# Performance work log

Measured on AMD Instinct MI355X. Metric: run time of the kernel, lower is better.

Reference implementation:

```python
import jax, jax.numpy as jnp
import numpy as np

EMB = 1024
HEADS = 16

def setup_inputs() -> dict:
    key = jax.random.key(0)
    ks = jax.random.split(key, 5)
    s = 1.0 / np.sqrt(EMB)
    x = jax.random.normal(ks[0], (2, 2048, EMB), dtype=jnp.float32)
    W_qkv = jax.random.normal(ks[1], (EMB, 3 * EMB), dtype=jnp.float32) * s
    b_qkv = jnp.zeros((3 * EMB,), dtype=jnp.float32)
    W_out = jax.random.normal(ks[2], (EMB, EMB), dtype=jnp.float32) * s
    b_out = jnp.zeros((EMB,), dtype=jnp.float32)
    return {"x": x, "W_qkv": W_qkv, "b_qkv": b_qkv, "W_out": W_out, "b_out": b_out}

def reference(x, W_qkv, b_qkv, W_out, b_out):
    B, N, C = x.shape
    H = HEADS
    D = C // H
    qkv = x @ W_qkv + b_qkv                      # [B,N,3C]
    qkv = qkv.reshape(B, N, 3, H, D)
    q, k, v = (qkv[:, :, i].transpose(0, 2, 1, 3) for i in range(3))  # [B,H,N,D]
    # NOTE: original scales by C**-0.5 (full embed dim), not head dim
    scale = C ** (-0.5)
    attn = jnp.einsum('bhnd,bhmd->bhnm', q, k) * scale
    attn = jax.nn.softmax(attn, axis=-1)
    out = jnp.einsum('bhnm,bhmd->bhnd', attn, v)  # [B,H,N,D]
    out = out.transpose(0, 2, 1, 3).reshape(B, N, C)
    return out @ W_out + b_out
```

## Files before the change

kernel.cpp:

```cpp
#include <hip/hip_runtime.h>
#include <hip/hip_bf16.h>
#include <cstdint>
#include <cstddef>

typedef __bf16 bf16;
typedef __bf16 bf16x4 __attribute__((ext_vector_type(4)));
typedef __bf16 bf16x8 __attribute__((ext_vector_type(8)));
typedef float f32x4 __attribute__((ext_vector_type(4)));
typedef float f32x16 __attribute__((ext_vector_type(16)));

#define LOG2E 1.4426950408889634f
#define QSCALE (0.03125f * LOG2E)

#define GLD16(gp, lp)                                                              \
  __builtin_amdgcn_global_load_lds((__attribute__((address_space(1))) void*)(gp),  \
                                   (__attribute__((address_space(3))) void*)(lp),  \
                                   16, 0, 0)

__global__ void k_prep(const float* __restrict__ x, const float* __restrict__ Wqkv,
                       const float* __restrict__ Wout, bf16* __restrict__ xb,
                       bf16* __restrict__ wqT, bf16* __restrict__ woT) {
  const int blk = blockIdx.x, tid = threadIdx.x;
  if (blk < 2048) {
    int i = (blk * 256 + tid) * 8;
    const float4* p = (const float4*)(x + i);
    float4 a = p[0], b = p[1];
    bf16x8 o;
    o[0] = (bf16)a.x; o[1] = (bf16)a.y; o[2] = (bf16)a.z; o[3] = (bf16)a.w;
    o[4] = (bf16)b.x; o[5] = (bf16)b.y; o[6] = (bf16)b.z; o[7] = (bf16)b.w;
    *(bf16x8*)(xb + i) = o;
    return;
  }
  const float* in;
  bf16* out;
  int R = 1024, C, bx, by;
  if (blk < 2048 + 3072) {
    in = Wqkv; out = wqT; C = 3072;
    bx = (blk - 2048) % 96; by = (blk - 2048) / 96;
  } else {
    in = Wout; out = woT; C = 1024;
    bx = (blk - 5120) % 32; by = (blk - 5120) / 32;
  }
  __shared__ float t[32][33];
  const int tx = tid & 31, ty = tid >> 5;
  int c0 = bx * 32, r0 = by * 32;
#pragma unroll
  for (int i = 0; i < 4; i++)
    t[ty + i * 8][tx] = in[(size_t)(r0 + ty + i * 8) * C + c0 + tx];
  __syncthreads();
#pragma unroll
  for (int i = 0; i < 4; i++)
    out[(size_t)(c0 + ty + i * 8) * R + r0 + tx] = (bf16)t[tx][ty + i * 8];
}

__global__ __launch_bounds__(256, 3) void k_gemm_qkv(
    const bf16* __restrict__ A, const bf16* __restrict__ Bt,
    const float* __restrict__ bias,
    bf16* __restrict__ qb, bf16* __restrict__ kb, bf16* __restrict__ vb) {
  __shared__ __align__(16) bf16 As[128 * 32];
  __shared__ __align__(16) bf16 Bs[128 * 32];
  const int tid = threadIdx.x;
  const int lane = tid & 63, w = tid >> 6;
  const int quad = lane >> 4, l16 = lane & 15;
  const int wm = (w >> 1) * 64, wn = (w & 1) * 64;
  const int bm = blockIdx.y * 128, bn = blockIdx.x * 128;
  f32x4 acc[4][4] = {};

  for (int kt = 0; kt < 1024; kt += 32) {
    __syncthreads();
#pragma unroll
    for (int p = 0; p < 2; p++) {
      int idx = p * 256 + tid;
      int row = idx >> 2, bq = idx & 3;
      int gb = (bq - ((row >> 1) & 3)) & 3;
      GLD16(A + (size_t)(bm + row) * 1024 + kt + gb * 8, As + idx * 8);
      GLD16(Bt + (size_t)(bn + row) * 1024 + kt + gb * 8, Bs + idx * 8);
    }
    __syncthreads();

    bf16x8 af[4], bfr[4];
#pragma unroll
    for (int mi = 0; mi < 4; mi++) {
      int row = wm + mi * 16 + l16;
      int bq = (quad + ((row >> 1) & 3)) & 3;
      af[mi] = *(const bf16x8*)(As + row * 32 + bq * 8);
    }
#pragma unroll
    for (int ni = 0; ni < 4; ni++) {
      int row = wn + ni * 16 + l16;
      int bq = (quad + ((row >> 1) & 3)) & 3;
      bfr[ni] = *(const bf16x8*)(Bs + row * 32 + bq * 8);
    }
#pragma unroll
    for (int mi = 0; mi < 4; mi++)
#pragma unroll
      for (int ni = 0; ni < 4; ni++)
        acc[mi][ni] =
            __builtin_amdgcn_mfma_f32_16x16x32_bf16(af[mi], bfr[ni], acc[mi][ni], 0, 0, 0);
  }

#pragma unroll
  for (int ni = 0; ni < 4; ni++) {
    int col = bn + wn + ni * 16 + l16;
    float bv = bias[col];
    int which = col >> 10, cc = col & 1023;
    int h = cc >> 6, d = cc & 63;
    if (which == 2) {
#pragma unroll
      for (int mi = 0; mi < 4; mi++) {
        int rowb = bm + wm + mi * 16 + quad * 4;
        int b = rowb >> 11, n0 = rowb & 2047;
        int n0p = (n0 & ~12) | ((n0 & 4) << 1) | ((n0 & 8) >> 1);
        bf16x4 vv;
#pragma unroll
        for (int r = 0; r < 4; r++) vv[r] = (bf16)(acc[mi][ni][r] + bv);
        *(bf16x4*)(vb + ((size_t)(b * 16 + h) * 64 + d) * 2048 + n0p) = vv;
      }
    } else {
#pragma unroll
      for (int mi = 0; mi < 4; mi++)
#pragma unroll
        for (int r = 0; r < 4; r++) {
          int row = bm + wm + mi * 16 + quad * 4 + r;
          int b = row >> 11, n = row & 2047;
          float v = acc[mi][ni][r] + bv;
          if (which == 0)
            qb[((size_t)(b * 16 + h) * 2048 + n) * 64 + d] = (bf16)(v * QSCALE);
          else
            kb[((size_t)(b * 16 + h) * 2048 + n) * 64 + d] = (bf16)v;
        }
    }
  }
}

__global__ __launch_bounds__(256, 2) void k_gemm_out(
    const bf16* __restrict__ A, const bf16* __restrict__ Bt,
    const float* __restrict__ bias, float* __restrict__ outF) {
  __shared__ __align__(16) bf16 As[64 * 32];
  __shared__ __align__(16) bf16 Bs[128 * 32];
  const int tid = threadIdx.x;
  const int lane = tid & 63, w = tid >> 6;
  const int quad = lane >> 4, l16 = lane & 15;
  const int wm = (w >> 1) * 32, wn = (w & 1) * 64;
  const int cid = (blockIdx.x & 7) * 64 + (blockIdx.x >> 3);
  const int bn = (cid & 7) * 128, bm = (cid >> 3) * 64;
  f32x4 acc[2][4] = {};

  for (int kt = 0; kt < 1024; kt += 32) {
    __syncthreads();
    {
      int idx = tid;
      int row = idx >> 2, bq = idx & 3;
      int gb = (bq - ((row >> 1) & 3)) & 3;
      GLD16(A + (size_t)(bm + row) * 1024 + kt + gb * 8, As + idx * 8);
    }
#pragma unroll
    for (int p = 0; p < 2; p++) {
      int idx = p * 256 + tid;
      int row = idx >> 2, bq = idx & 3;
      int gb = (bq - ((row >> 1) & 3)) & 3;
      GLD16(Bt + (size_t)(bn + row) * 1024 + kt + gb * 8, Bs + idx * 8);
    }
    __syncthreads();

    bf16x8 af[2], bfr[4];
#pragma unroll
    for (int mi = 0; mi < 2; mi++) {
      int row = wm + mi * 16 + l16;
      int bq = (quad + ((row >> 1) & 3)) & 3;
      af[mi] = *(const bf16x8*)(As + row * 32 + bq * 8);
    }
#pragma unroll
    for (int ni = 0; ni < 4; ni++) {
      int row = wn + ni * 16 + l16;
      int bq = (quad + ((row >> 1) & 3)) & 3;
      bfr[ni] = *(const bf16x8*)(Bs + row * 32 + bq * 8);
    }
#pragma unroll
    for (int mi = 0; mi < 2; mi++)
#pragma unroll
      for (int ni = 0; ni < 4; ni++)
        acc[mi][ni] =
            __builtin_amdgcn_mfma_f32_16x16x32_bf16(af[mi], bfr[ni], acc[mi][ni], 0, 0, 0);
  }

#pragma unroll
  for (int ni = 0; ni < 4; ni++) {
    int col = bn + wn + ni * 16 + l16;
    float bv = bias[col];
#pragma unroll
    for (int mi = 0; mi < 2; mi++)
#pragma unroll
      for (int r = 0; r < 4; r++) {
        int row = bm + wm + mi * 16 + quad * 4 + r;
        outF[(size_t)row * 1024 + col] = acc[mi][ni][r] + bv;
      }
  }
}

__global__ __launch_bounds__(256, 4) void k_flash(
    const bf16* __restrict__ Q, const bf16* __restrict__ K,
    const bf16* __restrict__ V, bf16* __restrict__ O) {
  __shared__ __align__(16) bf16 Kt[2][64 * 64];
  __shared__ __align__(16) bf16 Vt[2][64 * 64];
  const int tid = threadIdx.x;
  const int lane = tid & 63, w = tid >> 6;
  const int wq = w >> 1, wk = w & 1;
  const int l31 = lane & 31, h = lane >> 5;
  const int x7 = l31 & 7;
  const int cid = ((blockIdx.x & 7) << 7) | (blockIdx.x >> 3);
  const int qt = cid & 31, bh = cid >> 5;
  const bf16* qh = Q + (size_t)bh * 2048 * 64;
  const bf16* kh = K + (size_t)bh * 2048 * 64;
  const bf16* vh = V + (size_t)bh * 64 * 2048;
  const int qrow = qt * 64 + wq * 32 + l31;

  bf16x8 qf[4];
#pragma unroll
  for (int c4 = 0; c4 < 4; c4++)
    qf[c4] = *(const bf16x8*)(qh + (size_t)qrow * 64 + c4 * 16 + h * 8);

  bf16x8 ones;
#pragma unroll
  for (int j = 0; j < 8; j++) ones[j] = (bf16)1.0f;
  f32x16 z16 = {};

  f32x16 o0 = {}, o1 = {};
  f32x16 lacc = {};

  auto stage = [&](int kt2, int buf) {
#pragma unroll
    for (int pp = 0; pp < 2; pp++) {
      int idx = pp * 256 + tid;
      int row = idx >> 3, bq = idx & 7, gb = bq ^ (row & 7);
      GLD16(kh + (size_t)(kt2 * 64 + row) * 64 + gb * 8, &Kt[buf][idx * 8]);
      GLD16(vh + (size_t)row * 2048 + kt2 * 64 + gb * 8, &Vt[buf][idx * 8]);
    }
  };

  stage(0, 0);

  for (int t = 0; t < 32; t++) {
    const int p = t & 1;
    __syncthreads();
    if (t < 31) stage(t + 1, p ^ 1);

    f32x16 a;
    {
      const bf16* k0 = &Kt[p][0] + (wk * 32 + l31) * 64;
      __builtin_amdgcn_s_setprio(1);
#pragma unroll
      for (int c4 = 0; c4 < 4; c4++) {
        int off = ((2 * c4 + h) ^ x7) << 3;
        bf16x8 kf = *(const bf16x8*)(k0 + off);
        a = __builtin_amdgcn_mfma_f32_32x32x16_bf16(kf, qf[c4], c4 ? a : z16, 0, 0, 0);
      }
      __builtin_amdgcn_s_setprio(0);
    }

    {
      bf16x8 pf0, pf1;
#pragma unroll
      for (int j = 0; j < 8; j++) {
        pf0[j] = (bf16)__builtin_amdgcn_exp2f(a[j]);
        pf1[j] = (bf16)__builtin_amdgcn_exp2f(a[8 + j]);
      }
      const bf16* v0 = &Vt[p][0] + l31 * 64;
      const bf16* v1 = v0 + 32 * 64;
      int e0 = ((4 * wk + 0 + h) ^ x7) << 3;
      int e1 = ((4 * wk + 2 + h) ^ x7) << 3;
      bf16x8 vf00 = *(const bf16x8*)(v0 + e0);
      bf16x8 vf10 = *(const bf16x8*)(v1 + e0);
      bf16x8 vf01 = *(const bf16x8*)(v0 + e1);
      bf16x8 vf11 = *(const bf16x8*)(v1 + e1);
      __builtin_amdgcn_s_setprio(1);
      lacc = __builtin_amdgcn_mfma_f32_32x32x16_bf16(ones, pf0, lacc, 0, 0, 0);
      o0 = __builtin_amdgcn_mfma_f32_32x32x16_bf16(vf00, pf0, o0, 0, 0, 0);
      o1 = __builtin_amdgcn_mfma_f32_32x32x16_bf16(vf10, pf0, o1, 0, 0, 0);
      lacc = __builtin_amdgcn_mfma_f32_32x32x16_bf16(ones, pf1, lacc, 0, 0, 0);
      o0 = __builtin_amdgcn_mfma_f32_32x32x16_bf16(vf01, pf1, o0, 0, 0, 0);
      o1 = __builtin_amdgcn_mfma_f32_32x32x16_bf16(vf11, pf1, o1, 0, 0, 0);
      __builtin_amdgcn_s_setprio(0);
    }
  }

  __syncthreads();
  float* sc = (float*)&Kt[0][0];
  float* so0 = sc;
  float* so1 = sc + 2 * 64 * 17;
  float* sl  = sc + 4 * 64 * 17;
  if (wk == 1) {
    float* b0 = so0 + (wq * 64 + lane) * 17;
    float* b1 = so1 + (wq * 64 + lane) * 17;
#pragma unroll
    for (int i = 0; i < 16; i++) { b0[i] = o0[i]; b1[i] = o1[i]; }
    sl[wq * 64 + lane] = lacc[0];
  }
  __syncthreads();
  if (wk == 0) {
    float* b0 = so0 + (wq * 64 + lane) * 17;
    float* b1 = so1 + (wq * 64 + lane) * 17;
#pragma unroll
    for (int i = 0; i < 16; i++) { o0[i] += b0[i]; o1[i] += b1[i]; }
    float inv = 1.0f / (lacc[0] + sl[wq * 64 + lane]);
    const int bb = bh >> 4, hh = bh & 15;
    bf16* orow = O + ((size_t)bb * 2048 + qrow) * 1024 + hh * 64;
#pragma unroll
    for (int g = 0; g < 4; g++) {
      bf16x4 ov0, ov1;
#pragma unroll
      for (int r = 0; r < 4; r++) {
        ov0[r] = (bf16)(o0[4 * g + r] * inv);
        ov1[r] = (bf16)(o1[4 * g + r] * inv);
      }
      *(bf16x4*)(orow + 8 * g + 4 * h) = ov0;
      *(bf16x4*)(orow + 32 + 8 * g + 4 * h) = ov1;
    }
  }
}


extern "C" void kernel_launch(void* const* d_in, const int* in_sizes, int n_in,
                              void* d_out, int out_size, void* d_ws, size_t ws_size,
                              hipStream_t stream) {
  (void)in_sizes; (void)n_in; (void)out_size; (void)ws_size;
  const float* x    = (const float*)d_in[0];
  const float* Wqkv = (const float*)d_in[1];
  const float* bqkv = (const float*)d_in[2];
  const float* Wout = (const float*)d_in[3];
  const float* bout = (const float*)d_in[4];
  float* out = (float*)d_out;

  char* ws = (char*)d_ws;
  size_t off = 0;
  auto take = [&](size_t bytes) {
    char* p = ws + off;
    off += (bytes + 255) & ~(size_t)255;
    return p;
  };
  bf16* xb   = (bf16*)take((size_t)4096 * 1024 * 2);
  bf16* wqT  = (bf16*)take((size_t)3072 * 1024 * 2);
  bf16* woT  = (bf16*)take((size_t)1024 * 1024 * 2);
  bf16* qbuf = (bf16*)take((size_t)32 * 2048 * 64 * 2);
  bf16* kbuf = (bf16*)take((size_t)32 * 2048 * 64 * 2);
  bf16* vbuf = (bf16*)take((size_t)32 * 2048 * 64 * 2);
  bf16* aout = (bf16*)take((size_t)4096 * 1024 * 2);

  k_prep<<<6144, 256, 0, stream>>>(x, Wqkv, Wout, xb, wqT, woT);
  k_gemm_qkv<<<dim3(24, 32), 256, 0, stream>>>(xb, wqT, bqkv, qbuf, kbuf, vbuf);
  k_flash<<<dim3(1024), 256, 0, stream>>>(qbuf, kbuf, vbuf, aout);
  k_gemm_out<<<dim3(512), 256, 0, stream>>>(aout, woT, bout, out);
}
```

Baseline: 186.6 us.

## Double query rows per flash block and compute row sums on VALU

Each flash-attention block now covers 128 query rows instead of 64. Each wave holds two 32-row Q fragments, so every K/V tile staged in shared memory is reused across twice as many rows, and the grid shrinks to 512 blocks. The row-sum MFMA against a ones vector is dropped; the sum is accumulated with scalar adds and a lane shuffle instead. In exchange, register pressure roughly doubles (launch bounds relaxed to 2 blocks per SM), fewer blocks may underfill the GPU, and the epilogue now runs two reduction rounds with extra barriers.

```diff
diff --git a/kernel.cpp b/kernel.cpp
--- a/kernel.cpp
+++ b/kernel.cpp
@@ -198,7 +198,7 @@
   }
 }
 
-__global__ __launch_bounds__(256, 4) void k_flash(
+__global__ __launch_bounds__(256, 2) void k_flash(
     const bf16* __restrict__ Q, const bf16* __restrict__ K,
     const bf16* __restrict__ V, bf16* __restrict__ O) {
   __shared__ __align__(16) bf16 Kt[2][64 * 64];
@@ -208,25 +208,25 @@
   const int wq = w >> 1, wk = w & 1;
   const int l31 = lane & 31, h = lane >> 5;
   const int x7 = l31 & 7;
-  const int cid = ((blockIdx.x & 7) << 7) | (blockIdx.x >> 3);
-  const int qt = cid & 31, bh = cid >> 5;
+  const int cid = ((blockIdx.x & 7) << 6) | (blockIdx.x >> 3);
+  const int qt = cid & 15, bh = cid >> 4;
   const bf16* qh = Q + (size_t)bh * 2048 * 64;
   const bf16* kh = K + (size_t)bh * 2048 * 64;
   const bf16* vh = V + (size_t)bh * 64 * 2048;
-  const int qrow = qt * 64 + wq * 32 + l31;
-
-  bf16x8 qf[4];
-#pragma unroll
-  for (int c4 = 0; c4 < 4; c4++)
-    qf[c4] = *(const bf16x8*)(qh + (size_t)qrow * 64 + c4 * 16 + h * 8);
-
-  bf16x8 ones;
-#pragma unroll
-  for (int j = 0; j < 8; j++) ones[j] = (bf16)1.0f;
+  const int qrow0 = qt * 128 + wq * 64 + l31;
+
+  bf16x8 qf0[4], qf1[4];
+#pragma unroll
+  for (int c4 = 0; c4 < 4; c4++) {
+    qf0[c4] = *(const bf16x8*)(qh + (size_t)qrow0 * 64 + c4 * 16 + h * 8);
+    qf1[c4] = *(const bf16x8*)(qh + (size_t)(qrow0 + 32) * 64 + c4 * 16 + h * 8);
+  }
+
   f32x16 z16 = {};
 
-  f32x16 o0 = {}, o1 = {};
-  f32x16 lacc = {};
+  f32x16 oA0 = {}, oA1 = {};
+  f32x16 oB0 = {}, oB1 = {};
+  float ls0 = 0.f, ls1 = 0.f;
 
   auto stage = [&](int kt2, int buf) {
 #pragma unroll
@@ -245,7 +245,7 @@
     __syncthreads();
     if (t < 31) stage(t + 1, p ^ 1);
 
-    f32x16 a;
+    f32x16 a0, a1;
     {
       const bf16* k0 = &Kt[p][0] + (wk * 32 + l31) * 64;
       __builtin_amdgcn_s_setprio(1);
@@ -253,17 +253,25 @@
       for (int c4 = 0; c4 < 4; c4++) {
         int off = ((2 * c4 + h) ^ x7) << 3;
         bf16x8 kf = *(const bf16x8*)(k0 + off);
-        a = __builtin_amdgcn_mfma_f32_32x32x16_bf16(kf, qf[c4], c4 ? a : z16, 0, 0, 0);
+        a0 = __builtin_amdgcn_mfma_f32_32x32x16_bf16(kf, qf0[c4], c4 ? a0 : z16, 0, 0, 0);
+        a1 = __builtin_amdgcn_mfma_f32_32x32x16_bf16(kf, qf1[c4], c4 ? a1 : z16, 0, 0, 0);
       }
       __builtin_amdgcn_s_setprio(0);
     }
 
     {
-      bf16x8 pf0, pf1;
+      bf16x8 pf00, pf01, pf10, pf11;
 #pragma unroll
       for (int j = 0; j < 8; j++) {
-        pf0[j] = (bf16)__builtin_amdgcn_exp2f(a[j]);
-        pf1[j] = (bf16)__builtin_amdgcn_exp2f(a[8 + j]);
+        pf00[j] = (bf16)__builtin_amdgcn_exp2f(a0[j]);
+        pf01[j] = (bf16)__builtin_amdgcn_exp2f(a0[8 + j]);
+        pf10[j] = (bf16)__builtin_amdgcn_exp2f(a1[j]);
+        pf11[j] = (bf16)__builtin_amdgcn_exp2f(a1[8 + j]);
+      }
+#pragma unroll
+      for (int j = 0; j < 8; j++) {
+        ls0 += (float)pf00[j] + (float)pf01[j];
+        ls1 += (float)pf10[j] + (float)pf11[j];
       }
       const bf16* v0 = &Vt[p][0] + l31 * 64;
       const bf16* v1 = v0 + 32 * 64;
@@ -274,48 +282,57 @@
       bf16x8 vf01 = *(const bf16x8*)(v0 + e1);
       bf16x8 vf11 = *(const bf16x8*)(v1 + e1);
       __builtin_amdgcn_s_setprio(1);
-      lacc = __builtin_amdgcn_mfma_f32_32x32x16_bf16(ones, pf0, lacc, 0, 0, 0);
-      o0 = __builtin_amdgcn_mfma_f32_32x32x16_bf16(vf00, pf0, o0, 0, 0, 0);
-      o1 = __builtin_amdgcn_mfma_f32_32x32x16_bf16(vf10, pf0, o1, 0, 0, 0);
-      lacc = __builtin_amdgcn_mfma_f32_32x32x16_bf16(ones, pf1, lacc, 0, 0, 0);
-      o0 = __builtin_amdgcn_mfma_f32_32x32x16_bf16(vf01, pf1, o0, 0, 0, 0);
-      o1 = __builtin_amdgcn_mfma_f32_32x32x16_bf16(vf11, pf1, o1, 0, 0, 0);
+      oA0 = __builtin_amdgcn_mfma_f32_32x32x16_bf16(vf00, pf00, oA0, 0, 0, 0);
+      oA1 = __builtin_amdgcn_mfma_f32_32x32x16_bf16(vf10, pf00, oA1, 0, 0, 0);
+      oB0 = __builtin_amdgcn_mfma_f32_32x32x16_bf16(vf00, pf10, oB0, 0, 0, 0);
+      oB1 = __builtin_amdgcn_mfma_f32_32x32x16_bf16(vf10, pf10, oB1, 0, 0, 0);
+      oA0 = __builtin_amdgcn_mfma_f32_32x32x16_bf16(vf01, pf01, oA0, 0, 0, 0);
+      oA1 = __builtin_amdgcn_mfma_f32_32x32x16_bf16(vf11, pf01, oA1, 0, 0, 0);
+      oB0 = __builtin_amdgcn_mfma_f32_32x32x16_bf16(vf01, pf11, oB0, 0, 0, 0);
+      oB1 = __builtin_amdgcn_mfma_f32_32x32x16_bf16(vf11, pf11, oB1, 0, 0, 0);
       __builtin_amdgcn_s_setprio(0);
     }
   }
+
+  ls0 += __shfl_xor(ls0, 32, 64);
+  ls1 += __shfl_xor(ls1, 32, 64);
 
   __syncthreads();
   float* sc = (float*)&Kt[0][0];
-  float* so0 = sc;
-  float* so1 = sc + 2 * 64 * 17;
-  float* sl  = sc + 4 * 64 * 17;
-  if (wk == 1) {
-    float* b0 = so0 + (wq * 64 + lane) * 17;
-    float* b1 = so1 + (wq * 64 + lane) * 17;
-#pragma unroll
-    for (int i = 0; i < 16; i++) { b0[i] = o0[i]; b1[i] = o1[i]; }
-    sl[wq * 64 + lane] = lacc[0];
-  }
-  __syncthreads();
-  if (wk == 0) {
-    float* b0 = so0 + (wq * 64 + lane) * 17;
-    float* b1 = so1 + (wq * 64 + lane) * 17;
-#pragma unroll
-    for (int i = 0; i < 16; i++) { o0[i] += b0[i]; o1[i] += b1[i]; }
-    float inv = 1.0f / (lacc[0] + sl[wq * 64 + lane]);
-    const int bb = bh >> 4, hh = bh & 15;
-    bf16* orow = O + ((size_t)bb * 2048 + qrow) * 1024 + hh * 64;
-#pragma unroll
-    for (int g = 0; g < 4; g++) {
-      bf16x4 ov0, ov1;
-#pragma unroll
-      for (int r = 0; r < 4; r++) {
-        ov0[r] = (bf16)(o0[4 * g + r] * inv);
-        ov1[r] = (bf16)(o1[4 * g + r] * inv);
-      }
-      *(bf16x4*)(orow + 8 * g + 4 * h) = ov0;
-      *(bf16x4*)(orow + 32 + 8 * g + 4 * h) = ov1;
-    }
+  float* so = sc;
+  float* sl = sc + 2 * 64 * 33;
+  const int bb = bh >> 4, hh = bh & 15;
+#pragma unroll
+  for (int qs = 0; qs < 2; qs++) {
+    f32x16& po0 = qs ? oB0 : oA0;
+    f32x16& po1 = qs ? oB1 : oA1;
+    float lsq = qs ? ls1 : ls0;
+    if (wk == 1) {
+      float* b = so + (wq * 64 + lane) * 33;
+#pragma unroll
+      for (int i = 0; i < 16; i++) { b[i] = po0[i]; b[16 + i] = po1[i]; }
+      sl[wq * 64 + lane] = lsq;
+    }
+    __syncthreads();
+    if (wk == 0) {
+      float* b = so + (wq * 64 + lane) * 33;
+#pragma unroll
+      for (int i = 0; i < 16; i++) { po0[i] += b[i]; po1[i] += b[16 + i]; }
+      float inv = 1.0f / (lsq + sl[wq * 64 + lane]);
+      bf16* orow = O + ((size_t)bb * 2048 + qrow0 + qs * 32) * 1024 + hh * 64;
+#pragma unroll
+      for (int g = 0; g < 4; g++) {
+        bf16x4 ov0, ov1;
+#pragma unroll
+        for (int r = 0; r < 4; r++) {
+          ov0[r] = (bf16)(po0[4 * g + r] * inv);
+          ov1[r] = (bf16)(po1[4 * g + r] * inv);
+        }
+        *(bf16x4*)(orow + 8 * g + 4 * h) = ov0;
+        *(bf16x4*)(orow + 32 + 8 * g + 4 * h) = ov1;
+      }
+    }
+    __syncthreads();
   }
 }
 
@@ -348,6 +365,6 @@
 
   k_prep<<<6144, 256, 0, stream>>>(x, Wqkv, Wout, xb, wqT, woT);
   k_gemm_qkv<<<dim3(24, 32), 256, 0, stream>>>(xb, wqT, bqkv, qbuf, kbuf, vbuf);
-  k_flash<<<dim3(1024), 256, 0, stream>>>(qbuf, kbuf, vbuf, aout);
+  k_flash<<<dim3(512), 256, 0, stream>>>(qbuf, kbuf, vbuf, aout);
   k_gemm_out<<<dim3(512), 256, 0, stream>>>(aout, woT, bout, out);
 }
```

New measurement: 179.5 us. 3.8% less time.
